# Optimization experiments

Measured on AMD Instinct MI355X. Metric: run time of the kernel, lower is better.

Reference implementation:

```python
import jax, jax.numpy as jnp
import numpy as np

B, T, F, H, M = 64, 512, 32, 512, 20
O = (F + 2) * M  # (n_features + 2) * num_mixtures = 680


def _lstm_cell(x, h, c, w_ih, w_hh, b_ih, b_hh):
    # torch.nn.LSTMCell: gates ordered [i, f, g, o]
    gates = x @ w_ih.T + h @ w_hh.T + b_ih + b_hh
    i, f, g, o = jnp.split(gates, 4, axis=-1)
    i = jax.nn.sigmoid(i)
    f = jax.nn.sigmoid(f)
    g = jnp.tanh(g)
    o = jax.nn.sigmoid(o)
    c_new = f * c + i * g
    h_new = o * jnp.tanh(c_new)
    return h_new, c_new


def setup_inputs() -> dict:
    key = jax.random.key(0)
    ks = jax.random.split(key, 9)
    s1 = 1.0 / np.sqrt(H)  # torch LSTMCell init: U(-1/sqrt(hidden), 1/sqrt(hidden))
    s2 = 1.0 / np.sqrt(O)
    u = lambda k, shape, s: jax.random.uniform(k, shape, jnp.float32, -s, s)
    return {
        "data": jax.random.normal(ks[0], (B, T * F), jnp.float32),
        "W_ih1": u(ks[1], (4 * H, F), s1),
        "W_hh1": u(ks[2], (4 * H, H), s1),
        "b_ih1": u(ks[3], (4 * H,), s1),
        "b_hh1": u(ks[4], (4 * H,), s1),
        "W_ih2": u(ks[5], (4 * O, H), s2),
        "W_hh2": u(ks[6], (4 * O, O), s2),
        "b_ih2": u(ks[7], (4 * O,), s2),
        "b_hh2": u(ks[8], (4 * O,), s2),
    }


def reference(data, W_ih1, W_hh1, b_ih1, b_hh1, W_ih2, W_hh2, b_ih2, b_hh2):
    n_feat = W_ih1.shape[1]
    hid = W_hh1.shape[1]
    out_dim = W_hh2.shape[1]
    batch = data.shape[0]
    t_steps = data.shape[1] // n_feat
    xs = data.reshape(batch, t_steps, n_feat).transpose(1, 0, 2)  # (T, B, F)

    h1 = jnp.zeros((batch, hid), data.dtype)
    c1 = jnp.zeros((batch, hid), data.dtype)
    h2 = jnp.zeros((batch, out_dim), data.dtype)
    c2 = jnp.zeros((batch, out_dim), data.dtype)

    def step(carry, x_t):
        h1, c1, h2, c2 = carry
        h1, c1 = _lstm_cell(x_t, h1, c1, W_ih1, W_hh1, b_ih1, b_hh1)
        # NOTE: original feeds lstm1's CELL state c1 into lstm2, and collects
        # lstm2's CELL state (`output`) as the per-step output.
        h2, c2 = _lstm_cell(c1, h2, c2, W_ih2, W_hh2, b_ih2, b_hh2)
        return (h1, c1, h2, c2), c2

    _, outs = jax.lax.scan(step, (h1, c1, h2, c2), xs)  # (T, B, O)
    return outs.transpose(1, 0, 2)  # (B, T, O), matches torch.stack(outputs, 1)
```

## Files before the change

kernel.cpp:

```cpp
#include <hip/hip_runtime.h>
#include <math.h>

#define BB 64
#define TT 512
#define FF 32
#define HH 512
#define OO 680

typedef _Float16 half8 __attribute__((ext_vector_type(8)));
typedef float f32x4 __attribute__((ext_vector_type(4)));

#define H1SLAB 65536u
#define C1SLAB 65536u
#define H2SLAB 90112u
#define H1S_OFF 0u
#define C1S_OFF 131072u
#define H2S_OFF 262144u
#define BAR_OFF 442368u
#define MEMSET_BYTES 444928u

#define L1B  16
#define NBLK 59
#define LDS_BYTES 159744u

__device__ __forceinline__ float sigf(float x) { return 1.f / (1.f + expf(-x)); }

__device__ __forceinline__ unsigned long long aload8(const void* p) {
    return __hip_atomic_load((const unsigned long long*)p, __ATOMIC_RELAXED, __HIP_MEMORY_SCOPE_AGENT);
}
__device__ __forceinline__ void astore8(void* p, unsigned long long v) {
    __hip_atomic_store((unsigned long long*)p, v, __ATOMIC_RELAXED, __HIP_MEMORY_SCOPE_AGENT);
}
__device__ __forceinline__ half8 ld_act(const char* p) {
    union { unsigned long long u[2]; half8 h; } t;
    t.u[0] = aload8(p); t.u[1] = aload8(p + 8);
    return t.h;
}
__device__ __forceinline__ unsigned pack2h(float a, float b) {
    union { _Float16 h[2]; unsigned u; } t;
    t.h[0] = (_Float16)a; t.h[1] = (_Float16)b; return t.u;
}
__device__ __forceinline__ unsigned long long pack4h(float a, float b, float c, float d) {
    union { _Float16 h[4]; unsigned long long u; } t;
    t.h[0] = (_Float16)a; t.h[1] = (_Float16)b; t.h[2] = (_Float16)c; t.h[3] = (_Float16)d;
    return t.u;
}

__device__ __forceinline__ void gridbar(unsigned* bar, int blk, unsigned gen) {
    __syncthreads();
    if (threadIdx.x == 0) {
        __builtin_amdgcn_s_waitcnt(0);
        const int x = blk & 7;
        const unsigned gsz = (x < 3) ? 8u : 7u;
        unsigned* cnt  = bar + x * 32;
        unsigned* gcnt = bar + 256;
        unsigned* flag = bar + 320 + x * 32;
        const unsigned a = __hip_atomic_fetch_add(cnt, 1u, __ATOMIC_RELAXED, __HIP_MEMORY_SCOPE_AGENT);
        if (a == gsz - 1u) {
            __hip_atomic_store(cnt, 0u, __ATOMIC_RELAXED, __HIP_MEMORY_SCOPE_AGENT);
            const unsigned ga = __hip_atomic_fetch_add(gcnt, 1u, __ATOMIC_RELAXED, __HIP_MEMORY_SCOPE_AGENT);
            if (ga == 7u) {
                __hip_atomic_store(gcnt, 0u, __ATOMIC_RELAXED, __HIP_MEMORY_SCOPE_AGENT);
                #pragma unroll
                for (int r = 0; r < 8; ++r)
                    __hip_atomic_store(bar + 320 + r * 32, gen, __ATOMIC_RELAXED, __HIP_MEMORY_SCOPE_AGENT);
            }
        }
        while (__hip_atomic_load(flag, __ATOMIC_RELAXED, __HIP_MEMORY_SCOPE_AGENT) < gen)
            __builtin_amdgcn_s_sleep(2);
    }
    __syncthreads();
}

#define MFMA4(B, AT) \
    acc0 = __builtin_amdgcn_mfma_f32_16x16x32_f16(*(const half8*)((AT)       ), (B), acc0, 0, 0, 0); \
    acc1 = __builtin_amdgcn_mfma_f32_16x16x32_f16(*(const half8*)((AT) + 1024), (B), acc1, 0, 0, 0); \
    acc2 = __builtin_amdgcn_mfma_f32_16x16x32_f16(*(const half8*)((AT) + 2048), (B), acc2, 0, 0, 0); \
    acc3 = __builtin_amdgcn_mfma_f32_16x16x32_f16(*(const half8*)((AT) + 3072), (B), acc3, 0, 0, 0);

__global__ __launch_bounds__(512, 1)
void rnn_mfma(const float* __restrict__ data,
    const float* __restrict__ Wih1, const float* __restrict__ Whh1,
    const float* __restrict__ bih1, const float* __restrict__ bhh1,
    const float* __restrict__ Wih2, const float* __restrict__ Whh2,
    const float* __restrict__ bih2, const float* __restrict__ bhh2,
    char* __restrict__ wsb, float* __restrict__ out)
{
    extern __shared__ char lds[];
    const int tid = threadIdx.x, wv = tid >> 6, l = tid & 63;
    const int hi = l >> 4, lo = l & 15;
    const int blk = blockIdx.x;
    const bool isL1 = blk < L1B;
    unsigned* bar = (unsigned*)(wsb + BAR_OFF);
    const int bfrag = wv & 3;
    const int b = bfrag * 16 + lo;
    const int c0 = isL1 ? blk * 32 : (blk - L1B) * 16;

    if (isL1) {
        for (int u = tid; u < 136 * 256; u += 512) {
            const int tile = u >> 8, w = u & 255;
            const int ll = w >> 2, jj = w & 3;
            const int ks = tile >> 3, rest = tile & 7;
            const int gate = rest >> 1, chi = rest & 1;
            const int col = c0 + chi * 16 + (ll & 15);
            const int row = gate * HH + col;
            const int kk = ks * 32 + (ll >> 4) * 8 + jj * 2;
            const float v0 = (kk < FF)     ? Wih1[(size_t)row * FF + kk]     : Whh1[(size_t)row * HH + kk - FF];
            const float v1 = (kk + 1 < FF) ? Wih1[(size_t)row * FF + kk + 1] : Whh1[(size_t)row * HH + kk + 1 - FF];
            ((unsigned*)lds)[tile * 256 + w] = pack2h(v0, v1);
        }
    } else {
        for (int u = tid; u < 152 * 256; u += 512) {
            const int tile = u >> 8, w = u & 255;
            const int ll = w >> 2, jj = w & 3;
            const int ks = tile >> 2, gate = tile & 3;
            const int col = c0 + (ll & 15);
            const int kk = ks * 32 + (ll >> 4) * 8 + jj * 2;
            float v0 = 0.f, v1 = 0.f;
            if (col < OO) {
                if (kk < HH) v0 = Wih2[((size_t)gate * OO + col) * HH + kk];
                else if (kk < 1192) v0 = Whh2[((size_t)gate * OO + col) * OO + kk - HH];
                if (kk + 1 < HH) v1 = Wih2[((size_t)gate * OO + col) * HH + kk + 1];
                else if (kk + 1 < 1192) v1 = Whh2[((size_t)gate * OO + col) * OO + kk + 1 - HH];
            }
            ((unsigned*)lds)[tile * 256 + w] = pack2h(v0, v1);
        }
    }
    __syncthreads();

    float bs[2][4][4];
    if (wv < 4) {
        if (isL1) {
            #pragma unroll
            for (int chi = 0; chi < 2; ++chi)
                #pragma unroll
                for (int r = 0; r < 4; ++r) {
                    const int col = c0 + chi * 16 + hi * 4 + r;
                    #pragma unroll
                    for (int g = 0; g < 4; ++g)
                        bs[chi][r][g] = bih1[g * HH + col] + bhh1[g * HH + col];
                }
        } else {
            #pragma unroll
            for (int r = 0; r < 4; ++r) {
                const int col = c0 + hi * 4 + r;
                const bool ok = col < OO;
                #pragma unroll
                for (int g = 0; g < 4; ++g)
                    bs[0][r][g] = ok ? (bih2[g * OO + col] + bhh2[g * OO + col]) : 0.f;
            }
        }
    }

    const int gh = wv >> 2;
    float cr[8] = {0.f,0.f,0.f,0.f,0.f,0.f,0.f,0.f};
    f32x4 (*part1)[4][64] = (f32x4(*)[4][64])(lds + 136 * 1024);
    f32x4* part2 = (f32x4*)(lds + 152 * 1024);

    for (int s = 0; s <= TT; ++s) {
        const int A = s & 1, Bx = A ^ 1;
        const bool active = isL1 ? (s < TT) : (s >= 1);
        f32x4 acc0 = {0,0,0,0}, acc1 = {0,0,0,0}, acc2 = {0,0,0,0}, acc3 = {0,0,0,0};

        if (active) {
            if (isL1) {
                {
                    const float* xp = data + (size_t)b * (TT * FF) + (size_t)s * FF + hi * 8;
                    const float4 xa = *(const float4*)xp;
                    const float4 xb = *(const float4*)(xp + 4);
                    half8 bxf;
                    bxf[0] = (_Float16)xa.x; bxf[1] = (_Float16)xa.y;
                    bxf[2] = (_Float16)xa.z; bxf[3] = (_Float16)xa.w;
                    bxf[4] = (_Float16)xb.x; bxf[5] = (_Float16)xb.y;
                    bxf[6] = (_Float16)xb.z; bxf[7] = (_Float16)xb.w;
                    const char* at = lds + (size_t)(gh * 4) * 1024 + (size_t)l * 16;
                    MFMA4(bxf, at);
                }
                const char* h1p = wsb + H1S_OFF + (size_t)A * H1SLAB + (size_t)l * 16;
                #pragma unroll 4
                for (int ks = 1; ks <= 16; ++ks) {
                    const half8 bf = ld_act(h1p + (size_t)(((ks - 1) * 4 + bfrag)) * 1024);
                    const char* at = lds + (size_t)(ks * 8 + gh * 4) * 1024 + (size_t)l * 16;
                    MFMA4(bf, at);
                }
            } else {
                if (gh == 0) {
                    const char* c1p = wsb + C1S_OFF + (size_t)A * C1SLAB + (size_t)l * 16;
                    #pragma unroll 4
                    for (int ks = 0; ks < 16; ++ks) {
                        const half8 bf = ld_act(c1p + (size_t)(ks * 4 + bfrag) * 1024);
                        const char* at = lds + (size_t)ks * 4096 + (size_t)l * 16;
                        MFMA4(bf, at);
                    }
                    const char* h2p = wsb + H2S_OFF + (size_t)Bx * H2SLAB + (size_t)l * 16;
                    #pragma unroll
                    for (int ks = 16; ks < 19; ++ks) {
                        const half8 bf = ld_act(h2p + (size_t)((ks - 16) * 4 + bfrag) * 1024);
                        const char* at = lds + (size_t)ks * 4096 + (size_t)l * 16;
                        MFMA4(bf, at);
                    }
                } else {
                    const char* h2p = wsb + H2S_OFF + (size_t)Bx * H2SLAB + (size_t)l * 16;
                    #pragma unroll 4
                    for (int ks = 19; ks < 38; ++ks) {
                        const half8 bf = ld_act(h2p + (size_t)((ks - 16) * 4 + bfrag) * 1024);
                        const char* at = lds + (size_t)ks * 4096 + (size_t)l * 16;
                        MFMA4(bf, at);
                    }
                }
            }
        }

        if (isL1) {
            if (active) {
                if (wv >= 4) {
                    part1[wv - 4][0][l] = acc0; part1[wv - 4][1][l] = acc1;
                    part1[wv - 4][2][l] = acc2; part1[wv - 4][3][l] = acc3;
                }
                __syncthreads();
                if (wv < 4) {
                    #pragma unroll
                    for (int chi = 0; chi < 2; ++chi) {
                        const f32x4 o0 = (chi == 0) ? acc0 : acc1;
                        const f32x4 o1 = (chi == 0) ? acc2 : acc3;
                        const f32x4 p0 = part1[wv][chi][l];
                        const f32x4 p1 = part1[wv][2 + chi][l];
                        float cn[4], hn[4];
                        #pragma unroll
                        for (int r = 0; r < 4; ++r) {
                            const float ig = sigf(o0[r] + bs[chi][r][0]);
                            const float fg = sigf(o1[r] + bs[chi][r][1]);
                            const float gg = tanhf(p0[r] + bs[chi][r][2]);
                            const float og = sigf(p1[r] + bs[chi][r][3]);
                            const float c = fg * cr[chi * 4 + r] + ig * gg;
                            cr[chi * 4 + r] = c;
                            cn[r] = c; hn[r] = og * tanhf(c);
                        }
                        const int cc = c0 + chi * 16 + hi * 4;
                        const size_t aoff = (size_t)(((cc >> 5) * 4 + wv)) * 1024
                                          + (size_t)((((cc >> 3) & 3) * 16 + lo)) * 16
                                          + (size_t)((hi & 1) * 8);
                        astore8(wsb + H1S_OFF + (size_t)Bx * H1SLAB + aoff, pack4h(hn[0], hn[1], hn[2], hn[3]));
                        astore8(wsb + C1S_OFF + (size_t)Bx * C1SLAB + aoff, pack4h(cn[0], cn[1], cn[2], cn[3]));
                    }
                }
            }
        } else {
            if (active) {
                f32x4 pr0 = {0,0,0,0}, pr1 = {0,0,0,0}, pr2 = {0,0,0,0}, pr3 = {0,0,0,0};
                if (wv >= 4) part2[(wv - 4) * 64 + l] = acc0;
                __syncthreads();
                if (wv < 4) pr0 = part2[wv * 64 + l];
                __syncthreads();
                if (wv >= 4) part2[(wv - 4) * 64 + l] = acc1;
                __syncthreads();
                if (wv < 4) pr1 = part2[wv * 64 + l];
                __syncthreads();
                if (wv >= 4) part2[(wv - 4) * 64 + l] = acc2;
                __syncthreads();
                if (wv < 4) pr2 = part2[wv * 64 + l];
                __syncthreads();
                if (wv >= 4) part2[(wv - 4) * 64 + l] = acc3;
                __syncthreads();
                if (wv < 4) pr3 = part2[wv * 64 + l];
                if (wv < 4) {
                    const int u = s - 1;
                    float cn[4], hn[4];
                    #pragma unroll
                    for (int r = 0; r < 4; ++r) {
                        const float ig = sigf(acc0[r] + pr0[r] + bs[0][r][0]);
                        const float fg = sigf(acc1[r] + pr1[r] + bs[0][r][1]);
                        const float gg = tanhf(acc2[r] + pr2[r] + bs[0][r][2]);
                        const float og = sigf(acc3[r] + pr3[r] + bs[0][r][3]);
                        const float c = fg * cr[r] + ig * gg;
                        cr[r] = c;
                        cn[r] = c; hn[r] = og * tanhf(c);
                    }
                    const int cc = c0 + hi * 4;
                    if (cc < OO) {
                        const f32x4 q = {cn[0], cn[1], cn[2], cn[3]};
                        __builtin_nontemporal_store(q, (f32x4*)(out + (size_t)b * (TT * OO) + (size_t)u * OO + cc));
                        const size_t aoff = (size_t)(((cc >> 5) * 4 + wv)) * 1024
                                          + (size_t)((((cc >> 3) & 3) * 16 + lo)) * 16
                                          + (size_t)((hi & 1) * 8);
                        astore8(wsb + H2S_OFF + (size_t)A * H2SLAB + aoff, pack4h(hn[0], hn[1], hn[2], hn[3]));
                    }
                }
            }
        }
        gridbar(bar, blk, (unsigned)(s + 1));
    }
}

extern "C" void kernel_launch(void* const* d_in, const int* in_sizes, int n_in,
                              void* d_out, int out_size, void* d_ws, size_t ws_size,
                              hipStream_t stream)
{
    const float* data = (const float*)d_in[0];
    const float* Wih1 = (const float*)d_in[1];
    const float* Whh1 = (const float*)d_in[2];
    const float* bih1 = (const float*)d_in[3];
    const float* bhh1 = (const float*)d_in[4];
    const float* Wih2 = (const float*)d_in[5];
    const float* Whh2 = (const float*)d_in[6];
    const float* bih2 = (const float*)d_in[7];
    const float* bhh2 = (const float*)d_in[8];
    float* out = (float*)d_out;
    char* wsb  = (char*)d_ws;

    hipFuncSetAttribute((const void*)rnn_mfma, hipFuncAttributeMaxDynamicSharedMemorySize, (int)LDS_BYTES);
    hipMemsetAsync(wsb, 0, MEMSET_BYTES, stream);
    rnn_mfma<<<NBLK, 512, LDS_BYTES, stream>>>(data,
                                               Wih1, Whh1, bih1, bhh1,
                                               Wih2, Whh2, bih2, bhh2,
                                               wsb, out);
}
```

Before: 4.661 ms.

## Flatten grid barrier to monotonic group counters, defer output stores past barrier

Replaces the two-level reset-based grid barrier with monotonically increasing per-group counters. Each group's last arriver publishes a generation flag, and every block polls all eight flags, which removes the global counter hop and the counter resets. It also drops the explicit waitcnt before arrival and defers each step's output store to the next step, so the store is not on the barrier's critical path. The recurrent MFMA loops are also fully unrolled. The risks are memory-ordering: the h2 activation stores are no longer explicitly drained before arrival, and more polling traffic plus register pressure from the unrolling.

After: 4.895 ms. 5.0% more time.

```diff
diff --git a/kernel.cpp b/kernel.cpp
--- a/kernel.cpp
+++ b/kernel.cpp
@@ -49,25 +49,20 @@
 __device__ __forceinline__ void gridbar(unsigned* bar, int blk, unsigned gen) {
     __syncthreads();
     if (threadIdx.x == 0) {
-        __builtin_amdgcn_s_waitcnt(0);
         const int x = blk & 7;
         const unsigned gsz = (x < 3) ? 8u : 7u;
-        unsigned* cnt  = bar + x * 32;
-        unsigned* gcnt = bar + 256;
-        unsigned* flag = bar + 320 + x * 32;
+        unsigned* cnt = bar + x * 32;
         const unsigned a = __hip_atomic_fetch_add(cnt, 1u, __ATOMIC_RELAXED, __HIP_MEMORY_SCOPE_AGENT);
-        if (a == gsz - 1u) {
-            __hip_atomic_store(cnt, 0u, __ATOMIC_RELAXED, __HIP_MEMORY_SCOPE_AGENT);
-            const unsigned ga = __hip_atomic_fetch_add(gcnt, 1u, __ATOMIC_RELAXED, __HIP_MEMORY_SCOPE_AGENT);
-            if (ga == 7u) {
-                __hip_atomic_store(gcnt, 0u, __ATOMIC_RELAXED, __HIP_MEMORY_SCOPE_AGENT);
-                #pragma unroll
-                for (int r = 0; r < 8; ++r)
-                    __hip_atomic_store(bar + 320 + r * 32, gen, __ATOMIC_RELAXED, __HIP_MEMORY_SCOPE_AGENT);
-            }
-        }
-        while (__hip_atomic_load(flag, __ATOMIC_RELAXED, __HIP_MEMORY_SCOPE_AGENT) < gen)
-            __builtin_amdgcn_s_sleep(2);
+        if (a == gen * gsz - 1u)
+            __hip_atomic_store(bar + 256 + x * 32, gen, __ATOMIC_RELAXED, __HIP_MEMORY_SCOPE_AGENT);
+        for (;;) {
+            unsigned ok = 1u;
+            #pragma unroll
+            for (int r = 0; r < 8; ++r)
+                ok &= (__hip_atomic_load(bar + 256 + r * 32, __ATOMIC_RELAXED, __HIP_MEMORY_SCOPE_AGENT) >= gen) ? 1u : 0u;
+            if (ok) break;
+            __builtin_amdgcn_s_sleep(1);
+        }
     }
     __syncthreads();
 }
@@ -157,6 +152,9 @@
     f32x4 (*part1)[4][64] = (f32x4(*)[4][64])(lds + 136 * 1024);
     f32x4* part2 = (f32x4*)(lds + 152 * 1024);
 
+    f32x4 pend = {0,0,0,0};
+    float* pendP = nullptr;
+
     for (int s = 0; s <= TT; ++s) {
         const int A = s & 1, Bx = A ^ 1;
         const bool active = isL1 ? (s < TT) : (s >= 1);
@@ -177,7 +175,7 @@
                     MFMA4(bxf, at);
                 }
                 const char* h1p = wsb + H1S_OFF + (size_t)A * H1SLAB + (size_t)l * 16;
-                #pragma unroll 4
+                #pragma unroll
                 for (int ks = 1; ks <= 16; ++ks) {
                     const half8 bf = ld_act(h1p + (size_t)(((ks - 1) * 4 + bfrag)) * 1024);
                     const char* at = lds + (size_t)(ks * 8 + gh * 4) * 1024 + (size_t)l * 16;
@@ -185,8 +183,9 @@
                 }
             } else {
                 if (gh == 0) {
+                    if (pendP) { __builtin_nontemporal_store(pend, (f32x4*)pendP); pendP = nullptr; }
                     const char* c1p = wsb + C1S_OFF + (size_t)A * C1SLAB + (size_t)l * 16;
-                    #pragma unroll 4
+                    #pragma unroll
                     for (int ks = 0; ks < 16; ++ks) {
                         const half8 bf = ld_act(c1p + (size_t)(ks * 4 + bfrag) * 1024);
                         const char* at = lds + (size_t)ks * 4096 + (size_t)l * 16;
@@ -201,7 +200,7 @@
                     }
                 } else {
                     const char* h2p = wsb + H2S_OFF + (size_t)Bx * H2SLAB + (size_t)l * 16;
-                    #pragma unroll 4
+                    #pragma unroll
                     for (int ks = 19; ks < 38; ++ks) {
                         const half8 bf = ld_act(h2p + (size_t)((ks - 16) * 4 + bfrag) * 1024);
                         const char* at = lds + (size_t)ks * 4096 + (size_t)l * 16;
@@ -278,8 +277,8 @@
                     }
                     const int cc = c0 + hi * 4;
                     if (cc < OO) {
-                        const f32x4 q = {cn[0], cn[1], cn[2], cn[3]};
-                        __builtin_nontemporal_store(q, (f32x4*)(out + (size_t)b * (TT * OO) + (size_t)u * OO + cc));
+                        pend[0] = cn[0]; pend[1] = cn[1]; pend[2] = cn[2]; pend[3] = cn[3];
+                        pendP = out + (size_t)b * (TT * OO) + (size_t)u * OO + cc;
                         const size_t aoff = (size_t)(((cc >> 5) * 4 + wv)) * 1024
                                           + (size_t)((((cc >> 3) & 3) * 16 + lo)) * 16
                                           + (size_t)((hi & 1) * 8);
@@ -290,6 +289,9 @@
         }
         gridbar(bar, blk, (unsigned)(s + 1));
     }
+
+    if (!isL1 && wv < 4 && pendP)
+        __builtin_nontemporal_store(pend, (f32x4*)pendP);
 }
 
 extern "C" void kernel_launch(void* const* d_in, const int* in_sizes, int n_in,
```
